# Kernel tuning notes

Measured on AMD Instinct MI355X. Metric: run time of the kernel, lower is better.

The kernel has to match this reference:

```python
import jax, jax.numpy as jnp
import numpy as np

TOKENS, H, I = 2048, 3584, 18944


def setup_inputs() -> dict:
    key = jax.random.key(0)
    ks = jax.random.split(key, 8)
    x = jax.random.normal(ks[0], (TOKENS, H), dtype=jnp.float32)
    gate_w = jax.random.randint(ks[1], (I, H), -127, 128, dtype=jnp.int32).astype(jnp.int8)
    up_w = jax.random.randint(ks[2], (I, H), -127, 128, dtype=jnp.int32).astype(jnp.int8)
    down_w = jax.random.randint(ks[3], (H, I), -127, 128, dtype=jnp.int32).astype(jnp.int8)
    # realistic small per-tensor scales
    gate_w_scale = jnp.float32(0.01) * (jnp.float32(0.5) + jax.random.uniform(ks[4], ()))
    up_w_scale = jnp.float32(0.01) * (jnp.float32(0.5) + jax.random.uniform(ks[5], ()))
    down_w_scale = jnp.float32(0.01) * (jnp.float32(0.5) + jax.random.uniform(ks[6], ()))
    down_input_scale = jnp.float32(0.05) * (jnp.float32(0.5) + jax.random.uniform(ks[7], ()))
    return {"x": x, "gate_w": gate_w, "up_w": up_w, "down_w": down_w,
            "gate_w_scale": gate_w_scale, "up_w_scale": up_w_scale,
            "down_w_scale": down_w_scale, "down_input_scale": down_input_scale}


def _quant_per_token(x):
    # dynamic per-token symmetric int8 quantization
    s = jnp.max(jnp.abs(x), axis=-1, keepdims=True) / jnp.float32(127.0)
    s = jnp.maximum(s, jnp.float32(1e-8))
    q = jnp.clip(jnp.round(x / s), -127, 127).astype(jnp.int8)
    return q, s  # q: [T, K] int8, s: [T, 1] fp32


def _int8_gemm(q, w):
    # q: [T, K] int8, w: [N, K] int8 -> [T, N] int32 accumulate
    return jax.lax.dot(q, w.T, preferred_element_type=jnp.int32)


def reference(x, gate_w, up_w, down_w, gate_w_scale, up_w_scale,
              down_w_scale, down_input_scale):
    # fc1 (gate & up): per-token dynamic activation quant, shared quantized input
    qx, sx = _quant_per_token(x)
    gate = _int8_gemm(qx, gate_w).astype(jnp.float32) * sx * gate_w_scale  # [T, I]
    up = _int8_gemm(qx, up_w).astype(jnp.float32) * sx * up_w_scale        # [T, I]
    h = jax.nn.silu(gate) * up  # SwiGLU, fp32
    # fc2 (down): static per-tensor activation quant with stored input scale
    qh = jnp.clip(jnp.round(h / down_input_scale), -127, 127).astype(jnp.int8)
    out = _int8_gemm(qh, down_w).astype(jnp.float32) * (down_input_scale * down_w_scale)
    return out  # [T, H] fp32
```

## Files before the change

kernel.cpp:

```cpp
#include <hip/hip_runtime.h>
#include <stdint.h>

#define TOKENS 2048
#define H_DIM 3584
#define I_DIM 18944

typedef int v4i __attribute__((ext_vector_type(4)));

__device__ __forceinline__ void async_copy16(const void* g, void* lds) {
    __builtin_amdgcn_global_load_lds(
        (const __attribute__((address_space(1))) void*)g,
        (__attribute__((address_space(3))) void*)lds,
        16, 0, 0);
}


__global__ __launch_bounds__(256)
void pack_kernel(const int* __restrict__ src, int8_t* __restrict__ dst, int n16) {
    int i = blockIdx.x * 256 + threadIdx.x;
    if (i >= n16) return;
    const v4i* s = (const v4i*)src + (size_t)i * 4;
    union { int8_t b[16]; v4i v; } o;
#pragma unroll
    for (int j = 0; j < 4; ++j) {
        v4i w = s[j];
        o.b[j * 4 + 0] = (int8_t)w.x;
        o.b[j * 4 + 1] = (int8_t)w.y;
        o.b[j * 4 + 2] = (int8_t)w.z;
        o.b[j * 4 + 3] = (int8_t)w.w;
    }
    ((v4i*)dst)[i] = o.v;
}

__global__ __launch_bounds__(256)
void quant_x_kernel(const float* __restrict__ x,
                    int8_t* __restrict__ qx,
                    float* __restrict__ sx) {
    const int row = blockIdx.x;
    const float* xr = x + (size_t)row * H_DIM;
    float m = 0.0f;
    for (int j = threadIdx.x; j < H_DIM; j += 256)
        m = fmaxf(m, fabsf(xr[j]));
    for (int off = 32; off > 0; off >>= 1)
        m = fmaxf(m, __shfl_down(m, off, 64));
    __shared__ float wmax[4];
    if ((threadIdx.x & 63) == 0) wmax[threadIdx.x >> 6] = m;
    __syncthreads();
    float mm = fmaxf(fmaxf(wmax[0], wmax[1]), fmaxf(wmax[2], wmax[3]));
    float s = fmaxf(mm / 127.0f, 1e-8f);
    if (threadIdx.x == 0) sx[row] = s;
    for (int j = threadIdx.x; j < H_DIM; j += 256) {
        float q = rintf(xr[j] / s);
        q = fminf(fmaxf(q, -127.0f), 127.0f);
        qx[(size_t)row * H_DIM + j] = (int8_t)q;
    }
}

__global__ __launch_bounds__(256)
void fc1_kernel(const int8_t* __restrict__ qx,
                const float* __restrict__ sx,
                const int8_t* __restrict__ gw,
                const int8_t* __restrict__ uw,
                const float* __restrict__ gws,
                const float* __restrict__ uws,
                const float* __restrict__ dis,
                int8_t* __restrict__ qh) {
    __shared__ __align__(16) int8_t ldsA[128 * 64];
    __shared__ __align__(16) int8_t ldsG[64 * 64];
    __shared__ __align__(16) int8_t ldsU[64 * 64];

    const int tid  = threadIdx.x;
    const int wave = tid >> 6;
    const int lane = tid & 63;
    const int n0 = blockIdx.x * 64;
    const int m0 = blockIdx.y * 128;

    const int rowA  = tid >> 2;
    const int kOffB = (((tid & 3) ^ ((tid >> 3) & 3))) * 16;
    const int8_t* gA0 = qx + (size_t)(m0 + rowA) * H_DIM + kOffB;
    const int8_t* gA1 = qx + (size_t)(m0 + 64 + rowA) * H_DIM + kOffB;
    const int8_t* gG  = gw + (size_t)(n0 + rowA) * H_DIM + kOffB;
    const int8_t* gU  = uw + (size_t)(n0 + rowA) * H_DIM + kOffB;
    int8_t* lA0 = ldsA + tid * 16;
    int8_t* lA1 = ldsA + 4096 + tid * 16;
    int8_t* lG  = ldsG + tid * 16;
    int8_t* lU  = ldsU + tid * 16;

    const int fr = lane & 15;
    const int fq = lane >> 4;
    const int sw = fq ^ ((fr >> 1) & 3);
    const int8_t* rA0 = ldsA + (wave * 32 + fr) * 64 + sw * 16;
    const int8_t* rA1 = rA0 + 16 * 64;
    const int8_t* rG  = ldsG + fr * 64 + sw * 16;
    const int8_t* rU  = ldsU + fr * 64 + sw * 16;

    v4i accG[2][4] = {};
    v4i accU[2][4] = {};

    for (int k0 = 0; k0 < H_DIM; k0 += 64) {
        __syncthreads();
        async_copy16(gA0 + k0, lA0);
        async_copy16(gA1 + k0, lA1);
        async_copy16(gG + k0, lG);
        async_copy16(gU + k0, lU);
        __syncthreads();
        v4i a0 = *(const v4i*)rA0;
        v4i a1 = *(const v4i*)rA1;
#pragma unroll
        for (int n = 0; n < 4; ++n) {
            v4i bg = *(const v4i*)(rG + n * 16 * 64);
            v4i bu = *(const v4i*)(rU + n * 16 * 64);
            accG[0][n] = __builtin_amdgcn_mfma_i32_16x16x64_i8(a0, bg, accG[0][n], 0, 0, 0);
            accG[1][n] = __builtin_amdgcn_mfma_i32_16x16x64_i8(a1, bg, accG[1][n], 0, 0, 0);
            accU[0][n] = __builtin_amdgcn_mfma_i32_16x16x64_i8(a0, bu, accU[0][n], 0, 0, 0);
            accU[1][n] = __builtin_amdgcn_mfma_i32_16x16x64_i8(a1, bu, accU[1][n], 0, 0, 0);
        }
    }

    const float gscale = *gws;
    const float uscale = *uws;
    const float dis_v  = *dis;

#pragma unroll
    for (int m = 0; m < 2; ++m) {
#pragma unroll
        for (int r = 0; r < 4; ++r) {
            const int row = m0 + wave * 32 + m * 16 + fq * 4 + r;
            const float s  = sx[row];
            const float gs = s * gscale;
            const float us = s * uscale;
            const size_t base = (size_t)row * I_DIM + n0;
#pragma unroll
            for (int n = 0; n < 4; ++n) {
                float g = (float)accG[m][n][r] * gs;
                float u = (float)accU[m][n][r] * us;
                float h = (g / (1.0f + expf(-g))) * u;
                float q = rintf(h / dis_v);
                q = fminf(fmaxf(q, -127.0f), 127.0f);
                qh[base + n * 16 + fr] = (int8_t)q;
            }
        }
    }
}

__global__ __launch_bounds__(256)
void fc2_kernel(const int8_t* __restrict__ qh,
                const int8_t* __restrict__ dw,
                const float* __restrict__ dws,
                const float* __restrict__ dis,
                float* __restrict__ out) {
    __shared__ __align__(16) int8_t ldsA[128 * 64];
    __shared__ __align__(16) int8_t ldsW[64 * 64];

    const int tid  = threadIdx.x;
    const int wave = tid >> 6;
    const int lane = tid & 63;
    const int n0 = blockIdx.x * 64;
    const int m0 = blockIdx.y * 128;

    const int rowA  = tid >> 2;
    const int kOffB = (((tid & 3) ^ ((tid >> 3) & 3))) * 16;
    const int8_t* gA0 = qh + (size_t)(m0 + rowA) * I_DIM + kOffB;
    const int8_t* gA1 = qh + (size_t)(m0 + 64 + rowA) * I_DIM + kOffB;
    const int8_t* gW  = dw + (size_t)(n0 + rowA) * I_DIM + kOffB;
    int8_t* lA0 = ldsA + tid * 16;
    int8_t* lA1 = ldsA + 4096 + tid * 16;
    int8_t* lW  = ldsW + tid * 16;

    const int fr = lane & 15;
    const int fq = lane >> 4;
    const int sw = fq ^ ((fr >> 1) & 3);
    const int8_t* rA0 = ldsA + (wave * 32 + fr) * 64 + sw * 16;
    const int8_t* rA1 = rA0 + 16 * 64;
    const int8_t* rW  = ldsW + fr * 64 + sw * 16;

    v4i acc[2][4] = {};

    for (int k0 = 0; k0 < I_DIM; k0 += 64) {
        __syncthreads();
        async_copy16(gA0 + k0, lA0);
        async_copy16(gA1 + k0, lA1);
        async_copy16(gW + k0, lW);
        __syncthreads();
        v4i a0 = *(const v4i*)rA0;
        v4i a1 = *(const v4i*)rA1;
#pragma unroll
        for (int n = 0; n < 4; ++n) {
            v4i b = *(const v4i*)(rW + n * 16 * 64);
            acc[0][n] = __builtin_amdgcn_mfma_i32_16x16x64_i8(a0, b, acc[0][n], 0, 0, 0);
            acc[1][n] = __builtin_amdgcn_mfma_i32_16x16x64_i8(a1, b, acc[1][n], 0, 0, 0);
        }
    }

    const float sc = (*dis) * (*dws);
#pragma unroll
    for (int m = 0; m < 2; ++m)
#pragma unroll
        for (int n = 0; n < 4; ++n)
#pragma unroll
            for (int r = 0; r < 4; ++r) {
                const int row = m0 + wave * 32 + m * 16 + fq * 4 + r;
                const int col = n0 + n * 16 + fr;
                out[(size_t)row * H_DIM + col] = (float)acc[m][n][r] * sc;
            }
}

extern "C" void kernel_launch(void* const* d_in, const int* in_sizes, int n_in,
                              void* d_out, int out_size, void* d_ws, size_t ws_size,
                              hipStream_t stream) {
    const float* x    = (const float*)d_in[0];
    const int*   gw32 = (const int*)d_in[1];
    const int*   uw32 = (const int*)d_in[2];
    const int*   dw32 = (const int*)d_in[3];
    const float* gws  = (const float*)d_in[4];
    const float* uws  = (const float*)d_in[5];
    const float* dws  = (const float*)d_in[6];
    const float* dis  = (const float*)d_in[7];
    float* out = (float*)d_out;

    const size_t W = (size_t)I_DIM * H_DIM;
    int8_t* qx  = (int8_t*)d_ws;
    float*  sx  = (float*)((char*)d_ws + (size_t)TOKENS * H_DIM);
    int8_t* qh  = (int8_t*)((char*)d_ws + (size_t)TOKENS * H_DIM + TOKENS * 4);
    int8_t* gw8 = (int8_t*)((char*)d_ws + (size_t)TOKENS * H_DIM + TOKENS * 4
                            + (size_t)TOKENS * I_DIM);
    int8_t* uw8 = gw8 + W;
    int8_t* dw8 = uw8 + W;

    const int n16 = (int)(W / 16);
    const int packBlocks = (n16 + 255) / 256;
    pack_kernel<<<packBlocks, 256, 0, stream>>>(gw32, gw8, n16);
    pack_kernel<<<packBlocks, 256, 0, stream>>>(uw32, uw8, n16);
    pack_kernel<<<packBlocks, 256, 0, stream>>>(dw32, dw8, n16);

    quant_x_kernel<<<TOKENS, 256, 0, stream>>>(x, qx, sx);

    dim3 g1(I_DIM / 64, TOKENS / 128);
    fc1_kernel<<<g1, 256, 0, stream>>>(qx, sx, gw8, uw8, gws, uws, dis, qh);

    dim3 g2(H_DIM / 64, TOKENS / 128);
    fc2_kernel<<<g2, 256, 0, stream>>>(qh, dw8, dws, dis, out);
}
```

Measured before the change: 1.428 ms.

## Double K-tile depth to 128 in GEMMs and repack weights with coalesced int32 loads

Both GEMM kernels now stage 128 K-elements per iteration instead of 64, using 8-way XOR swizzle and issuing more async global-to-LDS copies per barrier pair. This halves the number of __syncthreads round-trips and gives more MFMA work per synchronization. The pack kernel is rewritten so each thread reads one int4 and writes one packed int32, improving coalescing. LDS use per block doubles, which may reduce occupancy.

```diff
diff --git a/kernel.cpp b/kernel.cpp
--- a/kernel.cpp
+++ b/kernel.cpp
@@ -16,20 +16,13 @@
 
 
 __global__ __launch_bounds__(256)
-void pack_kernel(const int* __restrict__ src, int8_t* __restrict__ dst, int n16) {
+void pack_kernel(const int* __restrict__ src, int8_t* __restrict__ dst, int n4) {
     int i = blockIdx.x * 256 + threadIdx.x;
-    if (i >= n16) return;
-    const v4i* s = (const v4i*)src + (size_t)i * 4;
-    union { int8_t b[16]; v4i v; } o;
-#pragma unroll
-    for (int j = 0; j < 4; ++j) {
-        v4i w = s[j];
-        o.b[j * 4 + 0] = (int8_t)w.x;
-        o.b[j * 4 + 1] = (int8_t)w.y;
-        o.b[j * 4 + 2] = (int8_t)w.z;
-        o.b[j * 4 + 3] = (int8_t)w.w;
-    }
-    ((v4i*)dst)[i] = o.v;
+    if (i >= n4) return;
+    v4i w = ((const v4i*)src)[i];
+    int packed = (w.x & 0xff) | ((w.y & 0xff) << 8) |
+                 ((w.z & 0xff) << 16) | (w.w << 24);
+    ((int*)dst)[i] = packed;
 }
 
 __global__ __launch_bounds__(256)
@@ -65,9 +58,9 @@
                 const float* __restrict__ uws,
                 const float* __restrict__ dis,
                 int8_t* __restrict__ qh) {
-    __shared__ __align__(16) int8_t ldsA[128 * 64];
-    __shared__ __align__(16) int8_t ldsG[64 * 64];
-    __shared__ __align__(16) int8_t ldsU[64 * 64];
+    __shared__ __align__(16) int8_t ldsA[128 * 128];
+    __shared__ __align__(16) int8_t ldsG[64 * 128];
+    __shared__ __align__(16) int8_t ldsU[64 * 128];
 
     const int tid  = threadIdx.x;
     const int wave = tid >> 6;
@@ -75,45 +68,46 @@
     const int n0 = blockIdx.x * 64;
     const int m0 = blockIdx.y * 128;
 
-    const int rowA  = tid >> 2;
-    const int kOffB = (((tid & 3) ^ ((tid >> 3) & 3))) * 16;
-    const int8_t* gA0 = qx + (size_t)(m0 + rowA) * H_DIM + kOffB;
-    const int8_t* gA1 = qx + (size_t)(m0 + 64 + rowA) * H_DIM + kOffB;
-    const int8_t* gG  = gw + (size_t)(n0 + rowA) * H_DIM + kOffB;
-    const int8_t* gU  = uw + (size_t)(n0 + rowA) * H_DIM + kOffB;
-    int8_t* lA0 = ldsA + tid * 16;
-    int8_t* lA1 = ldsA + 4096 + tid * 16;
-    int8_t* lG  = ldsG + tid * 16;
-    int8_t* lU  = ldsU + tid * 16;
+    const int rowS  = tid >> 3;
+    const int kOffS = (((tid & 7) ^ ((tid >> 3) & 7))) * 16;
+    const int8_t* gA = qx + (size_t)(m0 + rowS) * H_DIM + kOffS;
+    const int8_t* gG = gw + (size_t)(n0 + rowS) * H_DIM + kOffS;
+    const int8_t* gU = uw + (size_t)(n0 + rowS) * H_DIM + kOffS;
+    int8_t* lA = ldsA + tid * 16;
+    int8_t* lG = ldsG + tid * 16;
+    int8_t* lU = ldsU + tid * 16;
 
     const int fr = lane & 15;
     const int fq = lane >> 4;
-    const int sw = fq ^ ((fr >> 1) & 3);
-    const int8_t* rA0 = ldsA + (wave * 32 + fr) * 64 + sw * 16;
-    const int8_t* rA1 = rA0 + 16 * 64;
-    const int8_t* rG  = ldsG + fr * 64 + sw * 16;
-    const int8_t* rU  = ldsU + fr * 64 + sw * 16;
 
     v4i accG[2][4] = {};
     v4i accU[2][4] = {};
 
-    for (int k0 = 0; k0 < H_DIM; k0 += 64) {
-        __syncthreads();
-        async_copy16(gA0 + k0, lA0);
-        async_copy16(gA1 + k0, lA1);
-        async_copy16(gG + k0, lG);
-        async_copy16(gU + k0, lU);
-        __syncthreads();
-        v4i a0 = *(const v4i*)rA0;
-        v4i a1 = *(const v4i*)rA1;
-#pragma unroll
-        for (int n = 0; n < 4; ++n) {
-            v4i bg = *(const v4i*)(rG + n * 16 * 64);
-            v4i bu = *(const v4i*)(rU + n * 16 * 64);
-            accG[0][n] = __builtin_amdgcn_mfma_i32_16x16x64_i8(a0, bg, accG[0][n], 0, 0, 0);
-            accG[1][n] = __builtin_amdgcn_mfma_i32_16x16x64_i8(a1, bg, accG[1][n], 0, 0, 0);
-            accU[0][n] = __builtin_amdgcn_mfma_i32_16x16x64_i8(a0, bu, accU[0][n], 0, 0, 0);
-            accU[1][n] = __builtin_amdgcn_mfma_i32_16x16x64_i8(a1, bu, accU[1][n], 0, 0, 0);
+    for (int k0 = 0; k0 < H_DIM; k0 += 128) {
+        __syncthreads();
+#pragma unroll
+        for (int j = 0; j < 4; ++j)
+            async_copy16(gA + k0 + (size_t)(32 * j) * H_DIM, lA + j * 4096);
+#pragma unroll
+        for (int j = 0; j < 2; ++j) {
+            async_copy16(gG + k0 + (size_t)(32 * j) * H_DIM, lG + j * 4096);
+            async_copy16(gU + k0 + (size_t)(32 * j) * H_DIM, lU + j * 4096);
+        }
+        __syncthreads();
+#pragma unroll
+        for (int kh = 0; kh < 2; ++kh) {
+            const int sw = ((kh * 4 + fq) ^ (fr & 7)) * 16;
+            v4i a0 = *(const v4i*)(ldsA + (wave * 32 + fr) * 128 + sw);
+            v4i a1 = *(const v4i*)(ldsA + (wave * 32 + 16 + fr) * 128 + sw);
+#pragma unroll
+            for (int n = 0; n < 4; ++n) {
+                v4i bg = *(const v4i*)(ldsG + (n * 16 + fr) * 128 + sw);
+                v4i bu = *(const v4i*)(ldsU + (n * 16 + fr) * 128 + sw);
+                accG[0][n] = __builtin_amdgcn_mfma_i32_16x16x64_i8(a0, bg, accG[0][n], 0, 0, 0);
+                accG[1][n] = __builtin_amdgcn_mfma_i32_16x16x64_i8(a1, bg, accG[1][n], 0, 0, 0);
+                accU[0][n] = __builtin_amdgcn_mfma_i32_16x16x64_i8(a0, bu, accU[0][n], 0, 0, 0);
+                accU[1][n] = __builtin_amdgcn_mfma_i32_16x16x64_i8(a1, bu, accU[1][n], 0, 0, 0);
+            }
         }
     }
 
@@ -149,8 +143,8 @@
                 const float* __restrict__ dws,
                 const float* __restrict__ dis,
                 float* __restrict__ out) {
-    __shared__ __align__(16) int8_t ldsA[128 * 64];
-    __shared__ __align__(16) int8_t ldsW[64 * 64];
+    __shared__ __align__(16) int8_t ldsA[128 * 128];
+    __shared__ __align__(16) int8_t ldsW[64 * 128];
 
     const int tid  = threadIdx.x;
     const int wave = tid >> 6;
@@ -158,37 +152,38 @@
     const int n0 = blockIdx.x * 64;
     const int m0 = blockIdx.y * 128;
 
-    const int rowA  = tid >> 2;
-    const int kOffB = (((tid & 3) ^ ((tid >> 3) & 3))) * 16;
-    const int8_t* gA0 = qh + (size_t)(m0 + rowA) * I_DIM + kOffB;
-    const int8_t* gA1 = qh + (size_t)(m0 + 64 + rowA) * I_DIM + kOffB;
-    const int8_t* gW  = dw + (size_t)(n0 + rowA) * I_DIM + kOffB;
-    int8_t* lA0 = ldsA + tid * 16;
-    int8_t* lA1 = ldsA + 4096 + tid * 16;
-    int8_t* lW  = ldsW + tid * 16;
+    const int rowS  = tid >> 3;
+    const int kOffS = (((tid & 7) ^ ((tid >> 3) & 7))) * 16;
+    const int8_t* gA = qh + (size_t)(m0 + rowS) * I_DIM + kOffS;
+    const int8_t* gW = dw + (size_t)(n0 + rowS) * I_DIM + kOffS;
+    int8_t* lA = ldsA + tid * 16;
+    int8_t* lW = ldsW + tid * 16;
 
     const int fr = lane & 15;
     const int fq = lane >> 4;
-    const int sw = fq ^ ((fr >> 1) & 3);
-    const int8_t* rA0 = ldsA + (wave * 32 + fr) * 64 + sw * 16;
-    const int8_t* rA1 = rA0 + 16 * 64;
-    const int8_t* rW  = ldsW + fr * 64 + sw * 16;
 
     v4i acc[2][4] = {};
 
-    for (int k0 = 0; k0 < I_DIM; k0 += 64) {
-        __syncthreads();
-        async_copy16(gA0 + k0, lA0);
-        async_copy16(gA1 + k0, lA1);
-        async_copy16(gW + k0, lW);
-        __syncthreads();
-        v4i a0 = *(const v4i*)rA0;
-        v4i a1 = *(const v4i*)rA1;
-#pragma unroll
-        for (int n = 0; n < 4; ++n) {
-            v4i b = *(const v4i*)(rW + n * 16 * 64);
-            acc[0][n] = __builtin_amdgcn_mfma_i32_16x16x64_i8(a0, b, acc[0][n], 0, 0, 0);
-            acc[1][n] = __builtin_amdgcn_mfma_i32_16x16x64_i8(a1, b, acc[1][n], 0, 0, 0);
+    for (int k0 = 0; k0 < I_DIM; k0 += 128) {
+        __syncthreads();
+#pragma unroll
+        for (int j = 0; j < 4; ++j)
+            async_copy16(gA + k0 + (size_t)(32 * j) * I_DIM, lA + j * 4096);
+#pragma unroll
+        for (int j = 0; j < 2; ++j)
+            async_copy16(gW + k0 + (size_t)(32 * j) * I_DIM, lW + j * 4096);
+        __syncthreads();
+#pragma unroll
+        for (int kh = 0; kh < 2; ++kh) {
+            const int sw = ((kh * 4 + fq) ^ (fr & 7)) * 16;
+            v4i a0 = *(const v4i*)(ldsA + (wave * 32 + fr) * 128 + sw);
+            v4i a1 = *(const v4i*)(ldsA + (wave * 32 + 16 + fr) * 128 + sw);
+#pragma unroll
+            for (int n = 0; n < 4; ++n) {
+                v4i b = *(const v4i*)(ldsW + (n * 16 + fr) * 128 + sw);
+                acc[0][n] = __builtin_amdgcn_mfma_i32_16x16x64_i8(a0, b, acc[0][n], 0, 0, 0);
+                acc[1][n] = __builtin_amdgcn_mfma_i32_16x16x64_i8(a1, b, acc[1][n], 0, 0, 0);
+            }
         }
     }
 
@@ -227,11 +222,11 @@
     int8_t* uw8 = gw8 + W;
     int8_t* dw8 = uw8 + W;
 
-    const int n16 = (int)(W / 16);
-    const int packBlocks = (n16 + 255) / 256;
-    pack_kernel<<<packBlocks, 256, 0, stream>>>(gw32, gw8, n16);
-    pack_kernel<<<packBlocks, 256, 0, stream>>>(uw32, uw8, n16);
-    pack_kernel<<<packBlocks, 256, 0, stream>>>(dw32, dw8, n16);
+    const int n4 = (int)(W / 4);
+    const int packBlocks = (n4 + 255) / 256;
+    pack_kernel<<<packBlocks, 256, 0, stream>>>(gw32, gw8, n4);
+    pack_kernel<<<packBlocks, 256, 0, stream>>>(uw32, uw8, n4);
+    pack_kernel<<<packBlocks, 256, 0, stream>>>(dw32, dw8, n4);
 
     quant_x_kernel<<<TOKENS, 256, 0, stream>>>(x, qx, sx);
 
```

After: 1.281 ms. 1.12x faster.
